# Kernel tuning notes

Hardware: AMD Instinct MI355X
Metric: run time of the kernel (lower is better)

Reference implementation:

```python
import jax, jax.numpy as jnp
import numpy as np

N = 50000          # nodes
E = 800000         # edges (before self-loops)
D_IN, D_H, D_OUT = 128, 256, 256
SZ_C = 2           # channels
NUM_GRAPHS = 64
EPS = 1e-6


def setup_inputs() -> dict:
    key = jax.random.key(0)
    ks = jax.random.split(key, 12)
    x = jax.random.normal(ks[0], (N, D_IN), dtype=jnp.float32)
    edge = jax.random.randint(ks[1], (2, E), 0, N, dtype=jnp.int64)
    batch = jnp.sort(jax.random.randint(ks[2], (N,), 0, NUM_GRAPHS, dtype=jnp.int64))
    def glorot(k, shape):
        fan = shape[-2] + shape[-1]
        return jax.random.normal(k, shape, dtype=jnp.float32) * jnp.sqrt(2.0 / fan)
    W0 = glorot(ks[3], (SZ_C, D_IN, D_H)); b0 = jnp.zeros((SZ_C, D_H), jnp.float32)
    W1 = glorot(ks[4], (SZ_C, D_H, D_H));  b1 = jnp.zeros((SZ_C, D_H), jnp.float32)
    W2 = glorot(ks[5], (SZ_C, D_H, D_OUT)); b2 = jnp.zeros((SZ_C, D_OUT), jnp.float32)
    ln_w = jnp.ones((D_OUT,), jnp.float32)
    ln_b = jnp.zeros((D_OUT,), jnp.float32)
    return {"x": x, "edge": edge, "batch": batch,
            "W0": W0, "b0": b0, "W1": W1, "b1": b1, "W2": W2, "b2": b2,
            "ln_w": ln_w, "ln_b": ln_b}


def _gcn_conv(h, W, b, src, dst, norm):
    # PyG GCNConv: linear transform, then deg-normalized scatter-add, then bias
    h = h @ W                                  # [N, d_out]
    msg = h[src] * norm[:, None]               # [E+N, d_out] gathered messages
    agg = jax.ops.segment_sum(msg, dst, num_segments=N)
    return agg + b


def reference(x, edge, batch, W0, b0, W1, b1, W2, b2, ln_w, ln_b):
    # add self-loops (GCNConv default add_self_loops=True)
    loops = jnp.arange(N, dtype=edge.dtype)
    src = jnp.concatenate([edge[0], loops])
    dst = jnp.concatenate([edge[1], loops])
    # symmetric normalization: deg^{-1/2}[src] * deg^{-1/2}[dst], deg over targets
    deg = jax.ops.segment_sum(jnp.ones_like(dst, dtype=x.dtype), dst, num_segments=N)
    dinv = jnp.where(deg > 0, jax.lax.rsqrt(deg), 0.0)
    norm = dinv[src] * dinv[dst]

    channels = []
    for c in range(SZ_C):  # small fixed channel count
        h = x
        for (W, b) in ((W0[c], b0[c]), (W1[c], b1[c]), (W2[c], b2[c])):
            h = _gcn_conv(h, W, b, src, dst, norm)
            h = jax.nn.relu(h) + h  # residual: ReLU output + pre-ReLU input
        channels.append(h)
    channal = jnp.stack(channels)              # [sz_c, N, d_out]

    mean = channal.mean(-1, keepdims=True)
    var = channal.var(-1, keepdims=True)
    out = (channal - mean) * jax.lax.rsqrt(var + EPS) * ln_w + ln_b

    batchs = jnp.ones((SZ_C, 1), channal.dtype) * batch.astype(channal.dtype)[None, :]
    return out, batchs
```

## Files before the change

### kernel.cpp

```cpp
#include <hip/hip_runtime.h>
#include <hip/hip_bf16.h>

typedef __bf16 v8bf __attribute__((ext_vector_type(8)));
typedef float  v4f  __attribute__((ext_vector_type(4)));

constexpr int N_NODES = 50000;
constexpr int N_EDGES = 800000;
constexpr float LN_EPS = 1e-6f;
constexpr int ROW_TILES = N_NODES / 16;

__global__ void probe_kernel(const int* __restrict__ edge, int* __restrict__ flag) {
  int t = threadIdx.x;
  int nz = 0;
  for (int i = t * 2 + 1; i < 4096; i += 128) nz |= (edge[i] != 0);
  unsigned long long m = __ballot(nz);
  if (t == 0) flag[0] = (m == 0ull) ? 1 : 0;
}

__device__ __forceinline__ int ld_idx(const void* base, int i, int is64) {
  int v;
  if (is64) v = (int)((const long long*)base)[(long long)i];
  else      v = ((const int*)base)[i];
  if ((unsigned)v >= (unsigned)N_NODES) v = 0;
  return v;
}


__global__ void init_kernel(int* __restrict__ deg, int* __restrict__ gcount) {
  int i = blockIdx.x * 256 + threadIdx.x;
  if (i < N_NODES) deg[i] = 1;
  if (i == 0) gcount[0] = 0;
}

__global__ void count_kernel(const void* __restrict__ edge, const int* __restrict__ flag,
                             int* __restrict__ deg) {
  int e = blockIdx.x * 256 + threadIdx.x;
  if (e < N_EDGES) atomicAdd(&deg[ld_idx(edge, N_EDGES + e, flag[0])], 1);
}

__global__ __launch_bounds__(256) void block_offsets_kernel(
    const int* __restrict__ deg, int* __restrict__ gcount,
    int* __restrict__ rowstart, int* __restrict__ cursor, float* __restrict__ dinv) {
  __shared__ int ps[256];
  __shared__ int base_s;
  int tid = threadIdx.x;
  int node = blockIdx.x * 256 + tid;
  int d = (node < N_NODES) ? deg[node] : 1;
  int cnt = d - 1;
  ps[tid] = cnt;
  __syncthreads();
#pragma unroll
  for (int off = 1; off < 256; off <<= 1) {
    int v = (tid >= off) ? ps[tid - off] : 0;
    __syncthreads();
    ps[tid] += v;
    __syncthreads();
  }
  if (tid == 255) base_s = atomicAdd(gcount, ps[255]);
  __syncthreads();
  int start = base_s + ps[tid] - cnt;
  if (node < N_NODES) {
    rowstart[node] = start;
    cursor[node]   = start;
    dinv[node]     = rsqrtf((float)max(d, 1));
  }
}

__global__ void scatter_kernel(const void* __restrict__ edge, const int* __restrict__ flag,
                               int* __restrict__ cursor, int* __restrict__ csr_src) {
  int e = blockIdx.x * 256 + threadIdx.x;
  if (e >= N_EDGES) return;
  int f = flag[0];
  int s = ld_idx(edge, e, f);
  int d = ld_idx(edge, N_EDGES + e, f);
  int pos = atomicAdd(&cursor[d], 1);
  if ((unsigned)pos < (unsigned)N_EDGES) csr_src[pos] = s;
}

__global__ void pack_w_kernel(const float* __restrict__ W, __bf16* __restrict__ Wp) {
  int tid = blockIdx.x * 256 + threadIdx.x;
  int j    = tid & 7;
  int lane = (tid >> 3) & 63;
  int ct   = (tid >> 9) & 15;
  int kc   = tid >> 13;
  int k    = kc * 32 + ((lane >> 4) << 3) + j;
  int col  = ct * 16 + (lane & 15);
  Wp[tid] = (__bf16)W[k * 256 + col];
}

__global__ __launch_bounds__(256) void prescale_x_kernel(
    const float* __restrict__ x, const float* __restrict__ dinv, __bf16* __restrict__ xd) {
  int t = blockIdx.x * 256 + threadIdx.x;
  int node = t >> 4;
  int d0 = (t & 15) * 8;
  float di = dinv[node];
  v4f f0 = *(const v4f*)(x + (size_t)node * 128 + d0);
  v4f f1 = *(const v4f*)(x + (size_t)node * 128 + d0 + 4);
  v8bf o;
#pragma unroll
  for (int j = 0; j < 4; j++) { o[j] = (__bf16)(di * f0[j]); o[4 + j] = (__bf16)(di * f1[j]); }
  *(v8bf*)(xd + (size_t)node * 128 + d0) = o;
}

template <int D>
__global__ __launch_bounds__(256) void agg_kernel(
    const __bf16* __restrict__ Yd, const int* __restrict__ rowstart,
    const int* __restrict__ deg, const int* __restrict__ csr_src,
    const float* __restrict__ dinv, __bf16* __restrict__ U) {
  constexpr int SEGS = D / 128;
  int w = blockIdx.x * 4 + (threadIdx.x >> 6);
  int lane = threadIdx.x & 63;
  int node, seg;
  if (SEGS == 2) { node = w >> 1; seg = w & 1; } else { node = w; seg = 0; }
  int sub = lane >> 4;
  int d0 = seg * 128 + (lane & 15) * 8;

  int start = rowstart[node];
  int cnt = deg[node] - 1;
  start = max(0, min(start, N_EDGES));
  cnt = max(0, min(cnt, N_EDGES - start));
  int e = start, end = start + cnt;

  float di = dinv[node];
  v8bf ys = *(const v8bf*)(Yd + (unsigned)(node * D + d0));

  float a[8];
#pragma unroll
  for (int j = 0; j < 8; j++) a[j] = 0.f;

  for (; e + 16 <= end; e += 16) {
    int s0 = csr_src[e + sub];
    int s1 = csr_src[e + 4 + sub];
    int s2 = csr_src[e + 8 + sub];
    int s3 = csr_src[e + 12 + sub];
    if ((unsigned)s0 >= (unsigned)N_NODES) s0 = 0;
    if ((unsigned)s1 >= (unsigned)N_NODES) s1 = 0;
    if ((unsigned)s2 >= (unsigned)N_NODES) s2 = 0;
    if ((unsigned)s3 >= (unsigned)N_NODES) s3 = 0;
    v8bf y0 = *(const v8bf*)(Yd + (unsigned)(s0 * D + d0));
    v8bf y1 = *(const v8bf*)(Yd + (unsigned)(s1 * D + d0));
    v8bf y2 = *(const v8bf*)(Yd + (unsigned)(s2 * D + d0));
    v8bf y3 = *(const v8bf*)(Yd + (unsigned)(s3 * D + d0));
#pragma unroll
    for (int j = 0; j < 8; j++)
      a[j] += ((float)y0[j] + (float)y1[j]) + ((float)y2[j] + (float)y3[j]);
  }
  if (e + 8 <= end) {
    int s0 = csr_src[e + sub];
    int s1 = csr_src[e + 4 + sub];
    if ((unsigned)s0 >= (unsigned)N_NODES) s0 = 0;
    if ((unsigned)s1 >= (unsigned)N_NODES) s1 = 0;
    v8bf y0 = *(const v8bf*)(Yd + (unsigned)(s0 * D + d0));
    v8bf y1 = *(const v8bf*)(Yd + (unsigned)(s1 * D + d0));
#pragma unroll
    for (int j = 0; j < 8; j++) a[j] += (float)y0[j] + (float)y1[j];
    e += 8;
  }
  if (e + 4 <= end) {
    int s0 = csr_src[e + sub];
    if ((unsigned)s0 >= (unsigned)N_NODES) s0 = 0;
    v8bf y0 = *(const v8bf*)(Yd + (unsigned)(s0 * D + d0));
#pragma unroll
    for (int j = 0; j < 8; j++) a[j] += (float)y0[j];
    e += 4;
  }
  int rem = end - e;
  if (sub < rem) {
    int s0 = csr_src[e + sub];
    if ((unsigned)s0 >= (unsigned)N_NODES) s0 = 0;
    v8bf y0 = *(const v8bf*)(Yd + (unsigned)(s0 * D + d0));
#pragma unroll
    for (int j = 0; j < 8; j++) a[j] += (float)y0[j];
  }

#pragma unroll
  for (int off = 16; off < 64; off <<= 1)
#pragma unroll
    for (int j = 0; j < 8; j++) a[j] += __shfl_xor(a[j], off);

  if (sub == 0) {
    v8bf u;
#pragma unroll
    for (int j = 0; j < 8; j++) u[j] = (__bf16)(di * (a[j] + (float)ys[j]));
    *(v8bf*)(U + (unsigned)(node * D + d0)) = u;
  }
}

template <int K>
__global__ __launch_bounds__(256, 2) void gemm_mid_kernel(
    const __bf16* __restrict__ A, const __bf16* __restrict__ Wp,
    const float* __restrict__ bias, const float* __restrict__ dinv,
    __bf16* __restrict__ Hd) {
  constexpr int KC = K / 32;
  int lane = threadIdx.x & 63;
  int wave = threadIdx.x >> 6;

  v8bf bfrag[KC][4];
#pragma unroll
  for (int kc = 0; kc < KC; kc++)
#pragma unroll
    for (int c4 = 0; c4 < 4; c4++)
      bfrag[kc][c4] = *(const v8bf*)(Wp + ((size_t)((kc * 16 + wave * 4 + c4) * 64 + lane)) * 8);

  int arow = lane & 15;
  int akq = (lane >> 4) * 8;
  int ccol = wave * 64 + (lane & 15);
  float bcol[4];
#pragma unroll
  for (int c4 = 0; c4 < 4; c4++) bcol[c4] = bias[ccol + c4 * 16];

  for (int t = blockIdx.x; t < ROW_TILES; t += gridDim.x) {
    int row0 = t * 16;
    const __bf16* Ap = A + (size_t)(row0 + arow) * K + akq;
    v8bf af[KC];
#pragma unroll
    for (int kc = 0; kc < KC; kc++) af[kc] = *(const v8bf*)(Ap + kc * 32);

    v4f acc[4];
#pragma unroll
    for (int c4 = 0; c4 < 4; c4++) acc[c4] = (v4f){0.f, 0.f, 0.f, 0.f};
#pragma unroll
    for (int kc = 0; kc < KC; kc++)
#pragma unroll
      for (int c4 = 0; c4 < 4; c4++)
        acc[c4] = __builtin_amdgcn_mfma_f32_16x16x32_bf16(af[kc], bfrag[kc][c4], acc[c4], 0, 0, 0);

    int crow = row0 + ((lane >> 4) << 2);
    float dv[4];
#pragma unroll
    for (int r = 0; r < 4; r++) dv[r] = dinv[crow + r];
#pragma unroll
    for (int c4 = 0; c4 < 4; c4++)
#pragma unroll
      for (int r = 0; r < 4; r++) {
        float z = acc[c4][r] + bcol[c4];
        float h = z + fmaxf(z, 0.f);
        Hd[(size_t)(crow + r) * 256 + ccol + c4 * 16] = (__bf16)(dv[r] * h);
      }
  }
}

__global__ __launch_bounds__(256, 2) void gemm_final_kernel(
    const __bf16* __restrict__ A, const __bf16* __restrict__ Wp,
    const float* __restrict__ bias, const float* __restrict__ lnw,
    const float* __restrict__ lnb, float* __restrict__ out) {
  constexpr int KC = 8;
  __shared__ float ls1[4][16];
  __shared__ float ls2[4][16];
  int lane = threadIdx.x & 63;
  int wave = threadIdx.x >> 6;

  v8bf bfrag[KC][4];
#pragma unroll
  for (int kc = 0; kc < KC; kc++)
#pragma unroll
    for (int c4 = 0; c4 < 4; c4++)
      bfrag[kc][c4] = *(const v8bf*)(Wp + ((size_t)((kc * 16 + wave * 4 + c4) * 64 + lane)) * 8);

  int arow = lane & 15;
  int akq = (lane >> 4) * 8;
  int g = lane >> 4;
  int ccol = wave * 64 + (lane & 15);
  float bcol[4], wcol[4], lbcol[4];
#pragma unroll
  for (int c4 = 0; c4 < 4; c4++) {
    int col = ccol + c4 * 16;
    bcol[c4] = bias[col];
    wcol[c4] = lnw[col];
    lbcol[c4] = lnb[col];
  }

  for (int t = blockIdx.x; t < ROW_TILES; t += gridDim.x) {
    int row0 = t * 16;
    const __bf16* Ap = A + (size_t)(row0 + arow) * 256 + akq;
    v8bf af[KC];
#pragma unroll
    for (int kc = 0; kc < KC; kc++) af[kc] = *(const v8bf*)(Ap + kc * 32);

    v4f acc[4];
#pragma unroll
    for (int c4 = 0; c4 < 4; c4++) acc[c4] = (v4f){0.f, 0.f, 0.f, 0.f};
#pragma unroll
    for (int kc = 0; kc < KC; kc++)
#pragma unroll
      for (int c4 = 0; c4 < 4; c4++)
        acc[c4] = __builtin_amdgcn_mfma_f32_16x16x32_bf16(af[kc], bfrag[kc][c4], acc[c4], 0, 0, 0);

    float h[4][4];
#pragma unroll
    for (int c4 = 0; c4 < 4; c4++)
#pragma unroll
      for (int r = 0; r < 4; r++) {
        float z = acc[c4][r] + bcol[c4];
        h[c4][r] = z + fmaxf(z, 0.f);
      }

    float s1[4], s2[4];
#pragma unroll
    for (int r = 0; r < 4; r++) {
      s1[r] = 0.f; s2[r] = 0.f;
#pragma unroll
      for (int c4 = 0; c4 < 4; c4++) { s1[r] += h[c4][r]; s2[r] += h[c4][r] * h[c4][r]; }
    }
#pragma unroll
    for (int off = 1; off < 16; off <<= 1)
#pragma unroll
      for (int r = 0; r < 4; r++) {
        s1[r] += __shfl_xor(s1[r], off);
        s2[r] += __shfl_xor(s2[r], off);
      }
    if ((lane & 15) == 0) {
#pragma unroll
      for (int r = 0; r < 4; r++) { ls1[wave][g * 4 + r] = s1[r]; ls2[wave][g * 4 + r] = s2[r]; }
    }
    __syncthreads();
#pragma unroll
    for (int r = 0; r < 4; r++) {
      int row = g * 4 + r;
      float t1 = ls1[0][row] + ls1[1][row] + ls1[2][row] + ls1[3][row];
      float t2 = ls2[0][row] + ls2[1][row] + ls2[2][row] + ls2[3][row];
      float mean = t1 * (1.0f / 256.0f);
      float var = t2 * (1.0f / 256.0f) - mean * mean;
      float rstd = rsqrtf(fmaxf(var, 0.f) + LN_EPS);
#pragma unroll
      for (int c4 = 0; c4 < 4; c4++)
        out[(size_t)(row0 + row) * 256 + ccol + c4 * 16] =
            (h[c4][r] - mean) * rstd * wcol[c4] + lbcol[c4];
    }
    __syncthreads();
  }
}

__global__ void batchs_kernel(const void* __restrict__ batch, const int* __restrict__ flag,
                              float* __restrict__ ob) {
  int i = blockIdx.x * 256 + threadIdx.x;
  if (i >= N_NODES) return;
  int f = flag[0];
  int v;
  if (f) v = (int)((const long long*)batch)[i];
  else   v = ((const int*)batch)[i];
  float b = (float)v;
  ob[i] = b;
  ob[N_NODES + i] = b;
}


extern "C" void kernel_launch(void* const* d_in, const int* in_sizes, int n_in,
                              void* d_out, int out_size, void* d_ws, size_t ws_size,
                              hipStream_t stream) {
  const float* x    = (const float*)d_in[0];
  const void*  edge = d_in[1];
  const void*  batch= d_in[2];
  const float* W0   = (const float*)d_in[3];
  const float* b0   = (const float*)d_in[4];
  const float* W1   = (const float*)d_in[5];
  const float* b1   = (const float*)d_in[6];
  const float* W2   = (const float*)d_in[7];
  const float* b2   = (const float*)d_in[8];
  const float* lnw  = (const float*)d_in[9];
  const float* lnb  = (const float*)d_in[10];

  float* out_x = (float*)d_out;
  float* out_b = (float*)d_out + (size_t)2 * N_NODES * 256;

  char* p = (char*)d_ws;
  __bf16* Ubuf  = (__bf16*)p;  p += (size_t)N_NODES * 256 * 2;
  __bf16* xd    = Ubuf;
  __bf16* U0    = Ubuf + (size_t)N_NODES * 128;
  __bf16* U256  = Ubuf;
  int* csr_src  = (int*)p;     p += (size_t)N_EDGES * 4;
  int* deg      = (int*)p;     p += (size_t)N_NODES * 4;
  int* cursor   = (int*)p;     p += (size_t)N_NODES * 4;
  int* rowstart = (int*)p;     p += (size_t)N_NODES * 4;
  float* dinv   = (float*)p;   p += (size_t)N_NODES * 4;
  int* flag     = (int*)p;     p += 16;
  int* gcount   = (int*)p;     p += 16;
  __bf16* Wp    = (__bf16*)p;

  const int EB = (N_EDGES + 255) / 256;
  const int NB = (N_NODES + 255) / 256;

  probe_kernel<<<1, 64, 0, stream>>>((const int*)edge, flag);
  init_kernel<<<NB, 256, 0, stream>>>(deg, gcount);
  count_kernel<<<EB, 256, 0, stream>>>(edge, flag, deg);
  block_offsets_kernel<<<NB, 256, 0, stream>>>(deg, gcount, rowstart, cursor, dinv);
  scatter_kernel<<<EB, 256, 0, stream>>>(edge, flag, cursor, csr_src);

  for (int c = 0; c < 2; c++) {
    pack_w_kernel<<<128, 256, 0, stream>>>(W0 + (size_t)c * 128 * 256, Wp + c * 32768);
    pack_w_kernel<<<256, 256, 0, stream>>>(W1 + (size_t)c * 256 * 256, Wp + 65536 + c * 65536);
    pack_w_kernel<<<256, 256, 0, stream>>>(W2 + (size_t)c * 256 * 256, Wp + 196608 + c * 65536);
  }

  prescale_x_kernel<<<3125, 256, 0, stream>>>(x, dinv, xd);
  agg_kernel<128><<<N_NODES / 4, 256, 0, stream>>>(xd, rowstart, deg, csr_src, dinv, U0);

  for (int c = 0; c < 2; c++) {
    __bf16* Hd = (__bf16*)(out_x + (size_t)c * N_NODES * 256);
    gemm_mid_kernel<128><<<512, 256, 0, stream>>>(U0, Wp + c * 32768, b0 + c * 256, dinv, Hd);
  }

  for (int c = 0; c < 2; c++) {
    __bf16* Hd = (__bf16*)(out_x + (size_t)c * N_NODES * 256);
    agg_kernel<256><<<N_NODES / 2, 256, 0, stream>>>(Hd, rowstart, deg, csr_src, dinv, U256);
    gemm_mid_kernel<256><<<512, 256, 0, stream>>>(U256, Wp + 65536 + c * 65536, b1 + c * 256,
                                                  dinv, Hd);
    agg_kernel<256><<<N_NODES / 2, 256, 0, stream>>>(Hd, rowstart, deg, csr_src, dinv, U256);
    gemm_final_kernel<<<512, 256, 0, stream>>>(U256, Wp + 196608 + c * 65536, b2 + c * 256,
                                               lnw, lnb, out_x + (size_t)c * N_NODES * 256);
  }

  batchs_kernel<<<NB, 256, 0, stream>>>(batch, flag, out_b);
}
```

Before: 627.4 us.

## Aggregate both channels in one pass and merge weight packing kernels

Replaces per-channel aggregation with a dual-channel kernel that reads the CSR indices once and gathers rows from both channel feature buffers together. This amortises the index loads and loop overhead across the two channels. The buffer plan changes so that the second channel's aggregate lives in unused halves of the output buffer, and the final GEMMs are ordered so nothing is overwritten too early. The six weight-packing launches are folded into one kernel. The cost is more register pressure and a more fragile buffer-aliasing scheme.

```diff
diff --git a/kernel.cpp b/kernel.cpp
--- a/kernel.cpp
+++ b/kernel.cpp
@@ -77,15 +77,20 @@
   if ((unsigned)pos < (unsigned)N_EDGES) csr_src[pos] = s;
 }
 
-__global__ void pack_w_kernel(const float* __restrict__ W, __bf16* __restrict__ Wp) {
+__global__ void pack_all_kernel(const float* __restrict__ W0, const float* __restrict__ W1,
+                                const float* __restrict__ W2, __bf16* __restrict__ Wp) {
   int tid = blockIdx.x * 256 + threadIdx.x;
-  int j    = tid & 7;
-  int lane = (tid >> 3) & 63;
-  int ct   = (tid >> 9) & 15;
-  int kc   = tid >> 13;
+  const float* src; int local;
+  if (tid < 65536)       { src = W0 + (size_t)(tid >> 15) * (128 * 256); local = tid & 32767; }
+  else if (tid < 196608) { int t2 = tid - 65536;  src = W1 + (size_t)(t2 >> 16) * 65536; local = t2 & 65535; }
+  else                   { int t2 = tid - 196608; src = W2 + (size_t)(t2 >> 16) * 65536; local = t2 & 65535; }
+  int j    = local & 7;
+  int lane = (local >> 3) & 63;
+  int ct   = (local >> 9) & 15;
+  int kc   = local >> 13;
   int k    = kc * 32 + ((lane >> 4) << 3) + j;
   int col  = ct * 16 + (lane & 15);
-  Wp[tid] = (__bf16)W[k * 256 + col];
+  Wp[tid] = (__bf16)src[k * 256 + col];
 }
 
 __global__ __launch_bounds__(256) void prescale_x_kernel(
@@ -183,6 +188,85 @@
 #pragma unroll
     for (int j = 0; j < 8; j++) u[j] = (__bf16)(di * (a[j] + (float)ys[j]));
     *(v8bf*)(U + (unsigned)(node * D + d0)) = u;
+  }
+}
+
+__global__ __launch_bounds__(256) void agg_dual_kernel(
+    const __bf16* __restrict__ A0, const __bf16* __restrict__ A1,
+    const int* __restrict__ rowstart, const int* __restrict__ deg,
+    const int* __restrict__ csr_src, const float* __restrict__ dinv,
+    __bf16* __restrict__ U0, __bf16* __restrict__ U1) {
+  int w = blockIdx.x * 4 + (threadIdx.x >> 6);
+  int lane = threadIdx.x & 63;
+  int node = w >> 1, seg = w & 1;
+  int sub = lane >> 4;
+  int d0 = seg * 128 + (lane & 15) * 8;
+
+  int start = rowstart[node];
+  int cnt = deg[node] - 1;
+  start = max(0, min(start, N_EDGES));
+  cnt = max(0, min(cnt, N_EDGES - start));
+  int e = start, end = start + cnt;
+
+  float di = dinv[node];
+  v8bf ys0 = *(const v8bf*)(A0 + (unsigned)(node * 256 + d0));
+  v8bf ys1 = *(const v8bf*)(A1 + (unsigned)(node * 256 + d0));
+
+  float a0[8], a1[8];
+#pragma unroll
+  for (int j = 0; j < 8; j++) { a0[j] = 0.f; a1[j] = 0.f; }
+
+  for (; e + 8 <= end; e += 8) {
+    int s0 = csr_src[e + sub];
+    int s1 = csr_src[e + 4 + sub];
+    if ((unsigned)s0 >= (unsigned)N_NODES) s0 = 0;
+    if ((unsigned)s1 >= (unsigned)N_NODES) s1 = 0;
+    v8bf x00 = *(const v8bf*)(A0 + (unsigned)(s0 * 256 + d0));
+    v8bf x10 = *(const v8bf*)(A1 + (unsigned)(s0 * 256 + d0));
+    v8bf x01 = *(const v8bf*)(A0 + (unsigned)(s1 * 256 + d0));
+    v8bf x11 = *(const v8bf*)(A1 + (unsigned)(s1 * 256 + d0));
+#pragma unroll
+    for (int j = 0; j < 8; j++) {
+      a0[j] += (float)x00[j] + (float)x01[j];
+      a1[j] += (float)x10[j] + (float)x11[j];
+    }
+  }
+  if (e + 4 <= end) {
+    int s0 = csr_src[e + sub];
+    if ((unsigned)s0 >= (unsigned)N_NODES) s0 = 0;
+    v8bf x00 = *(const v8bf*)(A0 + (unsigned)(s0 * 256 + d0));
+    v8bf x10 = *(const v8bf*)(A1 + (unsigned)(s0 * 256 + d0));
+#pragma unroll
+    for (int j = 0; j < 8; j++) { a0[j] += (float)x00[j]; a1[j] += (float)x10[j]; }
+    e += 4;
+  }
+  int rem = end - e;
+  if (sub < rem) {
+    int s0 = csr_src[e + sub];
+    if ((unsigned)s0 >= (unsigned)N_NODES) s0 = 0;
+    v8bf x00 = *(const v8bf*)(A0 + (unsigned)(s0 * 256 + d0));
+    v8bf x10 = *(const v8bf*)(A1 + (unsigned)(s0 * 256 + d0));
+#pragma unroll
+    for (int j = 0; j < 8; j++) { a0[j] += (float)x00[j]; a1[j] += (float)x10[j]; }
+  }
+
+#pragma unroll
+  for (int off = 16; off < 64; off <<= 1)
+#pragma unroll
+    for (int j = 0; j < 8; j++) {
+      a0[j] += __shfl_xor(a0[j], off);
+      a1[j] += __shfl_xor(a1[j], off);
+    }
+
+  if (sub == 0) {
+    v8bf u0, u1;
+#pragma unroll
+    for (int j = 0; j < 8; j++) {
+      u0[j] = (__bf16)(di * (a0[j] + (float)ys0[j]));
+      u1[j] = (__bf16)(di * (a1[j] + (float)ys1[j]));
+    }
+    *(v8bf*)(U0 + (unsigned)(node * 256 + d0)) = u0;
+    *(v8bf*)(U1 + (unsigned)(node * 256 + d0)) = u1;
   }
 }
 
@@ -363,11 +447,15 @@
   float* out_x = (float*)d_out;
   float* out_b = (float*)d_out + (size_t)2 * N_NODES * 256;
 
+  __bf16* Hd0   = (__bf16*)out_x;
+  __bf16* Hd1   = (__bf16*)(out_x + (size_t)N_NODES * 256);
+  __bf16* R0hi  = (__bf16*)(out_x + (size_t)N_NODES * 128);
+  __bf16* R1hi  = (__bf16*)(out_x + (size_t)N_NODES * 256 + (size_t)N_NODES * 128);
+
   char* p = (char*)d_ws;
   __bf16* Ubuf  = (__bf16*)p;  p += (size_t)N_NODES * 256 * 2;
   __bf16* xd    = Ubuf;
   __bf16* U0    = Ubuf + (size_t)N_NODES * 128;
-  __bf16* U256  = Ubuf;
   int* csr_src  = (int*)p;     p += (size_t)N_EDGES * 4;
   int* deg      = (int*)p;     p += (size_t)N_NODES * 4;
   int* cursor   = (int*)p;     p += (size_t)N_NODES * 4;
@@ -386,29 +474,24 @@
   block_offsets_kernel<<<NB, 256, 0, stream>>>(deg, gcount, rowstart, cursor, dinv);
   scatter_kernel<<<EB, 256, 0, stream>>>(edge, flag, cursor, csr_src);
 
-  for (int c = 0; c < 2; c++) {
-    pack_w_kernel<<<128, 256, 0, stream>>>(W0 + (size_t)c * 128 * 256, Wp + c * 32768);
-    pack_w_kernel<<<256, 256, 0, stream>>>(W1 + (size_t)c * 256 * 256, Wp + 65536 + c * 65536);
-    pack_w_kernel<<<256, 256, 0, stream>>>(W2 + (size_t)c * 256 * 256, Wp + 196608 + c * 65536);
-  }
+  pack_all_kernel<<<1280, 256, 0, stream>>>(W0, W1, W2, Wp);
 
   prescale_x_kernel<<<3125, 256, 0, stream>>>(x, dinv, xd);
   agg_kernel<128><<<N_NODES / 4, 256, 0, stream>>>(xd, rowstart, deg, csr_src, dinv, U0);
 
-  for (int c = 0; c < 2; c++) {
-    __bf16* Hd = (__bf16*)(out_x + (size_t)c * N_NODES * 256);
-    gemm_mid_kernel<128><<<512, 256, 0, stream>>>(U0, Wp + c * 32768, b0 + c * 256, dinv, Hd);
-  }
-
-  for (int c = 0; c < 2; c++) {
-    __bf16* Hd = (__bf16*)(out_x + (size_t)c * N_NODES * 256);
-    agg_kernel<256><<<N_NODES / 2, 256, 0, stream>>>(Hd, rowstart, deg, csr_src, dinv, U256);
-    gemm_mid_kernel<256><<<512, 256, 0, stream>>>(U256, Wp + 65536 + c * 65536, b1 + c * 256,
-                                                  dinv, Hd);
-    agg_kernel<256><<<N_NODES / 2, 256, 0, stream>>>(Hd, rowstart, deg, csr_src, dinv, U256);
-    gemm_final_kernel<<<512, 256, 0, stream>>>(U256, Wp + 196608 + c * 65536, b2 + c * 256,
-                                               lnw, lnb, out_x + (size_t)c * N_NODES * 256);
-  }
+  gemm_mid_kernel<128><<<512, 256, 0, stream>>>(U0, Wp, b0, dinv, Hd0);
+  gemm_mid_kernel<128><<<512, 256, 0, stream>>>(U0, Wp + 32768, b0 + 256, dinv, Hd1);
+
+  agg_dual_kernel<<<N_NODES / 2, 256, 0, stream>>>(Hd0, Hd1, rowstart, deg, csr_src, dinv,
+                                                   Ubuf, R1hi);
+  gemm_mid_kernel<256><<<512, 256, 0, stream>>>(Ubuf, Wp + 65536, b1, dinv, Hd0);
+  gemm_mid_kernel<256><<<512, 256, 0, stream>>>(R1hi, Wp + 131072, b1 + 256, dinv, Hd1);
+
+  agg_dual_kernel<<<N_NODES / 2, 256, 0, stream>>>(Hd0, Hd1, rowstart, deg, csr_src, dinv,
+                                                   Ubuf, R0hi);
+  gemm_final_kernel<<<512, 256, 0, stream>>>(R0hi, Wp + 262144, b2 + 256, lnw, lnb,
+                                             out_x + (size_t)N_NODES * 256);
+  gemm_final_kernel<<<512, 256, 0, stream>>>(Ubuf, Wp + 196608, b2, lnw, lnb, out_x);
 
   batchs_kernel<<<NB, 256, 0, stream>>>(batch, flag, out_b);
 }
```

Result: faster. 614.0 us (-2.1%).

## Interleave both channels into 512-wide rows and aggregate them together

Applied to the files above, without the earlier changes.

Stores the two channels' hidden features side by side in one 512-wide bf16 row so each aggregation pass gathers both channels with a single CSR walk, one wave per node with 64 lanes covering 512 features. This halves the number of aggregation launches and the index reads. Each gathered row becomes a contiguous 1 KB read. The GEMMs take stride parameters so they can read and write into the interleaved buffer. The six weight-packing launches are merged into one. The final GEMMs are ordered carefully because the shared output buffer is overwritten in place, which adds aliasing risk.

```diff
diff --git a/kernel.cpp b/kernel.cpp
--- a/kernel.cpp
+++ b/kernel.cpp
@@ -77,15 +77,20 @@
   if ((unsigned)pos < (unsigned)N_EDGES) csr_src[pos] = s;
 }
 
-__global__ void pack_w_kernel(const float* __restrict__ W, __bf16* __restrict__ Wp) {
+__global__ void pack_all_kernel(const float* __restrict__ W0, const float* __restrict__ W1,
+                                const float* __restrict__ W2, __bf16* __restrict__ Wp) {
   int tid = blockIdx.x * 256 + threadIdx.x;
-  int j    = tid & 7;
-  int lane = (tid >> 3) & 63;
-  int ct   = (tid >> 9) & 15;
-  int kc   = tid >> 13;
+  const float* src; int local;
+  if (tid < 65536)       { src = W0 + (size_t)(tid >> 15) * (128 * 256); local = tid & 32767; }
+  else if (tid < 196608) { int t2 = tid - 65536;  src = W1 + (size_t)(t2 >> 16) * 65536; local = t2 & 65535; }
+  else                   { int t2 = tid - 196608; src = W2 + (size_t)(t2 >> 16) * 65536; local = t2 & 65535; }
+  int j    = local & 7;
+  int lane = (local >> 3) & 63;
+  int ct   = (local >> 9) & 15;
+  int kc   = local >> 13;
   int k    = kc * 32 + ((lane >> 4) << 3) + j;
   int col  = ct * 16 + (lane & 15);
-  Wp[tid] = (__bf16)W[k * 256 + col];
+  Wp[tid] = (__bf16)src[k * 256 + col];
 }
 
 __global__ __launch_bounds__(256) void prescale_x_kernel(
@@ -102,18 +107,14 @@
   *(v8bf*)(xd + (size_t)node * 128 + d0) = o;
 }
 
-template <int D>
-__global__ __launch_bounds__(256) void agg_kernel(
+__global__ __launch_bounds__(256) void agg128_kernel(
     const __bf16* __restrict__ Yd, const int* __restrict__ rowstart,
     const int* __restrict__ deg, const int* __restrict__ csr_src,
     const float* __restrict__ dinv, __bf16* __restrict__ U) {
-  constexpr int SEGS = D / 128;
-  int w = blockIdx.x * 4 + (threadIdx.x >> 6);
+  int node = blockIdx.x * 4 + (threadIdx.x >> 6);
   int lane = threadIdx.x & 63;
-  int node, seg;
-  if (SEGS == 2) { node = w >> 1; seg = w & 1; } else { node = w; seg = 0; }
   int sub = lane >> 4;
-  int d0 = seg * 128 + (lane & 15) * 8;
+  int d0 = (lane & 15) * 8;
 
   int start = rowstart[node];
   int cnt = deg[node] - 1;
@@ -122,7 +123,7 @@
   int e = start, end = start + cnt;
 
   float di = dinv[node];
-  v8bf ys = *(const v8bf*)(Yd + (unsigned)(node * D + d0));
+  v8bf ys = *(const v8bf*)(Yd + (unsigned)(node * 128 + d0));
 
   float a[8];
 #pragma unroll
@@ -137,10 +138,10 @@
     if ((unsigned)s1 >= (unsigned)N_NODES) s1 = 0;
     if ((unsigned)s2 >= (unsigned)N_NODES) s2 = 0;
     if ((unsigned)s3 >= (unsigned)N_NODES) s3 = 0;
-    v8bf y0 = *(const v8bf*)(Yd + (unsigned)(s0 * D + d0));
-    v8bf y1 = *(const v8bf*)(Yd + (unsigned)(s1 * D + d0));
-    v8bf y2 = *(const v8bf*)(Yd + (unsigned)(s2 * D + d0));
-    v8bf y3 = *(const v8bf*)(Yd + (unsigned)(s3 * D + d0));
+    v8bf y0 = *(const v8bf*)(Yd + (unsigned)(s0 * 128 + d0));
+    v8bf y1 = *(const v8bf*)(Yd + (unsigned)(s1 * 128 + d0));
+    v8bf y2 = *(const v8bf*)(Yd + (unsigned)(s2 * 128 + d0));
+    v8bf y3 = *(const v8bf*)(Yd + (unsigned)(s3 * 128 + d0));
 #pragma unroll
     for (int j = 0; j < 8; j++)
       a[j] += ((float)y0[j] + (float)y1[j]) + ((float)y2[j] + (float)y3[j]);
@@ -150,8 +151,8 @@
     int s1 = csr_src[e + 4 + sub];
     if ((unsigned)s0 >= (unsigned)N_NODES) s0 = 0;
     if ((unsigned)s1 >= (unsigned)N_NODES) s1 = 0;
-    v8bf y0 = *(const v8bf*)(Yd + (unsigned)(s0 * D + d0));
-    v8bf y1 = *(const v8bf*)(Yd + (unsigned)(s1 * D + d0));
+    v8bf y0 = *(const v8bf*)(Yd + (unsigned)(s0 * 128 + d0));
+    v8bf y1 = *(const v8bf*)(Yd + (unsigned)(s1 * 128 + d0));
 #pragma unroll
     for (int j = 0; j < 8; j++) a[j] += (float)y0[j] + (float)y1[j];
     e += 8;
@@ -159,7 +160,7 @@
   if (e + 4 <= end) {
     int s0 = csr_src[e + sub];
     if ((unsigned)s0 >= (unsigned)N_NODES) s0 = 0;
-    v8bf y0 = *(const v8bf*)(Yd + (unsigned)(s0 * D + d0));
+    v8bf y0 = *(const v8bf*)(Yd + (unsigned)(s0 * 128 + d0));
 #pragma unroll
     for (int j = 0; j < 8; j++) a[j] += (float)y0[j];
     e += 4;
@@ -168,7 +169,7 @@
   if (sub < rem) {
     int s0 = csr_src[e + sub];
     if ((unsigned)s0 >= (unsigned)N_NODES) s0 = 0;
-    v8bf y0 = *(const v8bf*)(Yd + (unsigned)(s0 * D + d0));
+    v8bf y0 = *(const v8bf*)(Yd + (unsigned)(s0 * 128 + d0));
 #pragma unroll
     for (int j = 0; j < 8; j++) a[j] += (float)y0[j];
   }
@@ -182,11 +183,89 @@
     v8bf u;
 #pragma unroll
     for (int j = 0; j < 8; j++) u[j] = (__bf16)(di * (a[j] + (float)ys[j]));
-    *(v8bf*)(U + (unsigned)(node * D + d0)) = u;
-  }
-}
-
-template <int K>
+    *(v8bf*)(U + (unsigned)(node * 128 + d0)) = u;
+  }
+}
+
+__global__ __launch_bounds__(256) void agg_fused512_kernel(
+    const __bf16* __restrict__ A,
+    const int* __restrict__ rowstart, const int* __restrict__ deg,
+    const int* __restrict__ csr_src, const float* __restrict__ dinv,
+    __bf16* __restrict__ U) {
+  int node = blockIdx.x * 4 + (threadIdx.x >> 6);
+  int lane = threadIdx.x & 63;
+  int d0 = lane * 8;
+
+  int start = rowstart[node];
+  int cnt = deg[node] - 1;
+  start = max(0, min(start, N_EDGES));
+  cnt = max(0, min(cnt, N_EDGES - start));
+  int e = start, end = start + cnt;
+
+  float di = dinv[node];
+  v8bf ys = *(const v8bf*)(A + (unsigned)(node * 512 + d0));
+
+  float a[8];
+#pragma unroll
+  for (int j = 0; j < 8; j++) a[j] = 0.f;
+
+  for (; e + 8 <= end; e += 8) {
+    int s0 = csr_src[e],     s1 = csr_src[e + 1];
+    int s2 = csr_src[e + 2], s3 = csr_src[e + 3];
+    int s4 = csr_src[e + 4], s5 = csr_src[e + 5];
+    int s6 = csr_src[e + 6], s7 = csr_src[e + 7];
+    if ((unsigned)s0 >= (unsigned)N_NODES) s0 = 0;
+    if ((unsigned)s1 >= (unsigned)N_NODES) s1 = 0;
+    if ((unsigned)s2 >= (unsigned)N_NODES) s2 = 0;
+    if ((unsigned)s3 >= (unsigned)N_NODES) s3 = 0;
+    if ((unsigned)s4 >= (unsigned)N_NODES) s4 = 0;
+    if ((unsigned)s5 >= (unsigned)N_NODES) s5 = 0;
+    if ((unsigned)s6 >= (unsigned)N_NODES) s6 = 0;
+    if ((unsigned)s7 >= (unsigned)N_NODES) s7 = 0;
+    v8bf y0 = *(const v8bf*)(A + (unsigned)(s0 * 512 + d0));
+    v8bf y1 = *(const v8bf*)(A + (unsigned)(s1 * 512 + d0));
+    v8bf y2 = *(const v8bf*)(A + (unsigned)(s2 * 512 + d0));
+    v8bf y3 = *(const v8bf*)(A + (unsigned)(s3 * 512 + d0));
+    v8bf y4 = *(const v8bf*)(A + (unsigned)(s4 * 512 + d0));
+    v8bf y5 = *(const v8bf*)(A + (unsigned)(s5 * 512 + d0));
+    v8bf y6 = *(const v8bf*)(A + (unsigned)(s6 * 512 + d0));
+    v8bf y7 = *(const v8bf*)(A + (unsigned)(s7 * 512 + d0));
+#pragma unroll
+    for (int j = 0; j < 8; j++)
+      a[j] += (((float)y0[j] + (float)y1[j]) + ((float)y2[j] + (float)y3[j])) +
+              (((float)y4[j] + (float)y5[j]) + ((float)y6[j] + (float)y7[j]));
+  }
+  if (e + 4 <= end) {
+    int s0 = csr_src[e],     s1 = csr_src[e + 1];
+    int s2 = csr_src[e + 2], s3 = csr_src[e + 3];
+    if ((unsigned)s0 >= (unsigned)N_NODES) s0 = 0;
+    if ((unsigned)s1 >= (unsigned)N_NODES) s1 = 0;
+    if ((unsigned)s2 >= (unsigned)N_NODES) s2 = 0;
+    if ((unsigned)s3 >= (unsigned)N_NODES) s3 = 0;
+    v8bf y0 = *(const v8bf*)(A + (unsigned)(s0 * 512 + d0));
+    v8bf y1 = *(const v8bf*)(A + (unsigned)(s1 * 512 + d0));
+    v8bf y2 = *(const v8bf*)(A + (unsigned)(s2 * 512 + d0));
+    v8bf y3 = *(const v8bf*)(A + (unsigned)(s3 * 512 + d0));
+#pragma unroll
+    for (int j = 0; j < 8; j++)
+      a[j] += ((float)y0[j] + (float)y1[j]) + ((float)y2[j] + (float)y3[j]);
+    e += 4;
+  }
+  for (; e < end; e++) {
+    int s0 = csr_src[e];
+    if ((unsigned)s0 >= (unsigned)N_NODES) s0 = 0;
+    v8bf y0 = *(const v8bf*)(A + (unsigned)(s0 * 512 + d0));
+#pragma unroll
+    for (int j = 0; j < 8; j++) a[j] += (float)y0[j];
+  }
+
+  v8bf u;
+#pragma unroll
+  for (int j = 0; j < 8; j++) u[j] = (__bf16)(di * (a[j] + (float)ys[j]));
+  *(v8bf*)(U + (unsigned)(node * 512 + d0)) = u;
+}
+
+template <int K, int LDA, int LDO>
 __global__ __launch_bounds__(256, 2) void gemm_mid_kernel(
     const __bf16* __restrict__ A, const __bf16* __restrict__ Wp,
     const float* __restrict__ bias, const float* __restrict__ dinv,
@@ -211,7 +290,7 @@
 
   for (int t = blockIdx.x; t < ROW_TILES; t += gridDim.x) {
     int row0 = t * 16;
-    const __bf16* Ap = A + (size_t)(row0 + arow) * K + akq;
+    const __bf16* Ap = A + (size_t)(row0 + arow) * LDA + akq;
     v8bf af[KC];
 #pragma unroll
     for (int kc = 0; kc < KC; kc++) af[kc] = *(const v8bf*)(Ap + kc * 32);
@@ -235,7 +314,7 @@
       for (int r = 0; r < 4; r++) {
         float z = acc[c4][r] + bcol[c4];
         float h = z + fmaxf(z, 0.f);
-        Hd[(size_t)(crow + r) * 256 + ccol + c4 * 16] = (__bf16)(dv[r] * h);
+        Hd[(size_t)(crow + r) * LDO + ccol + c4 * 16] = (__bf16)(dv[r] * h);
       }
   }
 }
@@ -245,6 +324,7 @@
     const float* __restrict__ bias, const float* __restrict__ lnw,
     const float* __restrict__ lnb, float* __restrict__ out) {
   constexpr int KC = 8;
+  constexpr int LDA = 512;
   __shared__ float ls1[4][16];
   __shared__ float ls2[4][16];
   int lane = threadIdx.x & 63;
@@ -272,7 +352,7 @@
 
   for (int t = blockIdx.x; t < ROW_TILES; t += gridDim.x) {
     int row0 = t * 16;
-    const __bf16* Ap = A + (size_t)(row0 + arow) * 256 + akq;
+    const __bf16* Ap = A + (size_t)(row0 + arow) * LDA + akq;
     v8bf af[KC];
 #pragma unroll
     for (int kc = 0; kc < KC; kc++) af[kc] = *(const v8bf*)(Ap + kc * 32);
@@ -363,11 +443,13 @@
   float* out_x = (float*)d_out;
   float* out_b = (float*)d_out + (size_t)2 * N_NODES * 256;
 
+  __bf16* UC  = (__bf16*)out_x;
+  __bf16* HdC = (__bf16*)(out_x + (size_t)N_NODES * 256);
+
   char* p = (char*)d_ws;
   __bf16* Ubuf  = (__bf16*)p;  p += (size_t)N_NODES * 256 * 2;
   __bf16* xd    = Ubuf;
   __bf16* U0    = Ubuf + (size_t)N_NODES * 128;
-  __bf16* U256  = Ubuf;
   int* csr_src  = (int*)p;     p += (size_t)N_EDGES * 4;
   int* deg      = (int*)p;     p += (size_t)N_NODES * 4;
   int* cursor   = (int*)p;     p += (size_t)N_NODES * 4;
@@ -386,29 +468,24 @@
   block_offsets_kernel<<<NB, 256, 0, stream>>>(deg, gcount, rowstart, cursor, dinv);
   scatter_kernel<<<EB, 256, 0, stream>>>(edge, flag, cursor, csr_src);
 
-  for (int c = 0; c < 2; c++) {
-    pack_w_kernel<<<128, 256, 0, stream>>>(W0 + (size_t)c * 128 * 256, Wp + c * 32768);
-    pack_w_kernel<<<256, 256, 0, stream>>>(W1 + (size_t)c * 256 * 256, Wp + 65536 + c * 65536);
-    pack_w_kernel<<<256, 256, 0, stream>>>(W2 + (size_t)c * 256 * 256, Wp + 196608 + c * 65536);
-  }
+  pack_all_kernel<<<1280, 256, 0, stream>>>(W0, W1, W2, Wp);
 
   prescale_x_kernel<<<3125, 256, 0, stream>>>(x, dinv, xd);
-  agg_kernel<128><<<N_NODES / 4, 256, 0, stream>>>(xd, rowstart, deg, csr_src, dinv, U0);
-
-  for (int c = 0; c < 2; c++) {
-    __bf16* Hd = (__bf16*)(out_x + (size_t)c * N_NODES * 256);
-    gemm_mid_kernel<128><<<512, 256, 0, stream>>>(U0, Wp + c * 32768, b0 + c * 256, dinv, Hd);
-  }
-
-  for (int c = 0; c < 2; c++) {
-    __bf16* Hd = (__bf16*)(out_x + (size_t)c * N_NODES * 256);
-    agg_kernel<256><<<N_NODES / 2, 256, 0, stream>>>(Hd, rowstart, deg, csr_src, dinv, U256);
-    gemm_mid_kernel<256><<<512, 256, 0, stream>>>(U256, Wp + 65536 + c * 65536, b1 + c * 256,
-                                                  dinv, Hd);
-    agg_kernel<256><<<N_NODES / 2, 256, 0, stream>>>(Hd, rowstart, deg, csr_src, dinv, U256);
-    gemm_final_kernel<<<512, 256, 0, stream>>>(U256, Wp + 196608 + c * 65536, b2 + c * 256,
-                                               lnw, lnb, out_x + (size_t)c * N_NODES * 256);
-  }
+  agg128_kernel<<<N_NODES / 4, 256, 0, stream>>>(xd, rowstart, deg, csr_src, dinv, U0);
+
+  gemm_mid_kernel<128, 128, 512><<<512, 256, 0, stream>>>(U0, Wp, b0, dinv, HdC);
+  gemm_mid_kernel<128, 128, 512><<<512, 256, 0, stream>>>(U0, Wp + 32768, b0 + 256, dinv,
+                                                          HdC + 256);
+
+  agg_fused512_kernel<<<N_NODES / 4, 256, 0, stream>>>(HdC, rowstart, deg, csr_src, dinv, UC);
+  gemm_mid_kernel<256, 512, 512><<<512, 256, 0, stream>>>(UC, Wp + 65536, b1, dinv, HdC);
+  gemm_mid_kernel<256, 512, 512><<<512, 256, 0, stream>>>(UC + 256, Wp + 131072, b1 + 256,
+                                                          dinv, HdC + 256);
+
+  agg_fused512_kernel<<<N_NODES / 4, 256, 0, stream>>>(HdC, rowstart, deg, csr_src, dinv, UC);
+  gemm_final_kernel<<<512, 256, 0, stream>>>(UC + 256, Wp + 262144, b2 + 256, lnw, lnb,
+                                             out_x + (size_t)N_NODES * 256);
+  gemm_final_kernel<<<512, 256, 0, stream>>>(UC, Wp + 196608, b2, lnw, lnb, out_x);
 
   batchs_kernel<<<NB, 256, 0, stream>>>(batch, flag, out_b);
 }
```

Measured after the change: 622.4 us. About the same (-0.8%).
